# Kernel optimization log

Measured on AMD Instinct MI355X. Metric: run time of the kernel, lower is better.

## Reference

```python
import jax, jax.numpy as jnp
import numpy as np

TOP_K = 32
OBS_RADIUS = 1.0
N = 4096
IN_DIM = 4


def setup_inputs() -> dict:
    key = jax.random.key(0)
    ks = jax.random.split(key, 10)
    s = 0.05
    return {
        "states": jax.random.normal(ks[0], (N, 4), jnp.float32),
        "goals": jax.random.normal(ks[1], (N, 2), jnp.float32),
        "W1": jax.random.normal(ks[2], (64, IN_DIM + 1), jnp.float32) * s,
        "b1": jnp.zeros((64,), jnp.float32),
        "W2": jax.random.normal(ks[3], (128, 64), jnp.float32) * s,
        "b2": jnp.zeros((128,), jnp.float32),
        "Wd1": jax.random.normal(ks[4], (64, 132), jnp.float32) * s,
        "bd1": jnp.zeros((64,), jnp.float32),
        "Wd2": jax.random.normal(ks[5], (128, 64), jnp.float32) * s,
        "bd2": jnp.zeros((128,), jnp.float32),
        "Wd3": jax.random.normal(ks[6], (64, 128), jnp.float32) * s,
        "bd3": jnp.zeros((64,), jnp.float32),
        "Wd4": jax.random.normal(ks[7], (4, 64), jnp.float32) * s,
        "bd4": jnp.zeros((4,), jnp.float32),
    }


def reference(states, goals, W1, b1, W2, b2, Wd1, bd1, Wd2, bd2, Wd3, bd3, Wd4, bd4):
    n = states.shape[0]
    dt = states.dtype
    # pairwise relative states + one-hot self indicator -> [N, N, 5]
    x = states[:, None, :] - states[None, :, :]
    x = jnp.concatenate([x, jnp.eye(n, dtype=dt)[:, :, None]], axis=2)
    # remove_distant_agents: keep TOP_K nearest neighbors by planar distance
    d = jnp.sqrt(jnp.sum(x[:, :, :2] ** 2, axis=2) + 1e-4)  # [N, N]
    _, idx = jax.lax.top_k(-d, TOP_K)                        # [N, K]
    xk = jnp.take_along_axis(x, idx[:, :, None], axis=1)     # [N, K, 5]
    # observation-radius mask (torch reshape [N,K,1]->[N,1,K] == transpose here)
    dist = jnp.linalg.norm(xk[:, :, :2], axis=2)             # [N, K]
    mask = (dist < OBS_RADIUS).astype(dt).reshape(n, 1, TOP_K)
    # NOTE: original uses a raw reshape [N,K,5]->[N,5,K] (not a transpose); match it
    h = xk.reshape(n, IN_DIM + 1, TOP_K)
    # pointwise (kernel-1) conv stack 5 -> 64 -> 128
    h = jax.nn.relu(jnp.einsum('oc,ncp->nop', W1, h) + b1[None, :, None])
    h = jax.nn.relu(jnp.einsum('oc,ncp->nop', W2, h) + b2[None, :, None])
    # original does torch.max(...)[1]: ARGMAX indices, promoted to float by cat
    x_local = jnp.argmax(h * mask, axis=2).astype(dt)        # [N, 128]
    rel = states[:, :2] - goals
    feat = jnp.concatenate([x_local, rel, states[:, 2:]], axis=1)  # [N, 132]
    z = jax.nn.relu(feat @ Wd1.T + bd1)
    z = jax.nn.relu(z @ Wd2.T + bd2)
    z = jax.nn.relu(z @ Wd3.T + bd3)
    z = z @ Wd4.T + bd4
    k = 2.0 * jax.nn.sigmoid(z) + 0.2                        # [N, 4] gains
    state = jnp.concatenate([rel, states[:, 2:]], axis=1)    # [N, 4]
    a_x = -(k[:, 0] * state[:, 0] + k[:, 1] * state[:, 2])
    a_y = -(k[:, 2] * state[:, 1] + k[:, 3] * state[:, 3])
    return jnp.stack([a_x, a_y], axis=1)                     # [N, 2]
```

## Files before the change

### kernel.cpp

```cpp
#include <hip/hip_runtime.h>
#include <math.h>

#define NAGENT 4096
#define TOPK 32
#define AGB 4
#define DAGB 16
#define CANDCAP 2048

__global__ __launch_bounds__(256) void topk_kernel(
    const float* __restrict__ states, int* __restrict__ idx_out)
{
    const int i = blockIdx.x;
    const int t = threadIdx.x;
    __shared__ unsigned int hist[1024];
    __shared__ unsigned int ps[256];
    __shared__ unsigned int ps2[32];
    __shared__ unsigned long long cand[CANDCAP];
    __shared__ int ccount;
    __shared__ unsigned int cutB;

    #pragma unroll
    for (int u = 0; u < 4; ++u) hist[t + u * 256] = 0u;
    if (t == 0) ccount = 0;

    const float4 si = ((const float4*)states)[i];
    __syncthreads();

    unsigned int mybits[16];
    #pragma unroll
    for (int u = 0; u < 16; ++u) {
        int j = t + u * 256;
        float4 sj = ((const float4*)states)[j];
        float dx = __fsub_rn(si.x, sj.x);
        float dy = __fsub_rn(si.y, sj.y);
        float s  = __fadd_rn(__fadd_rn(__fmul_rn(dx, dx), __fmul_rn(dy, dy)), 1e-4f);
        float dv = sqrtf(s);
        mybits[u] = __float_as_uint(dv);
        unsigned int bin = (unsigned int)(dv * 256.0f);
        if (bin > 1023u) bin = 1023u;
        atomicAdd(&hist[bin], 1u);
    }
    __syncthreads();

    ps[t] = hist[t * 4 + 0] + hist[t * 4 + 1] + hist[t * 4 + 2] + hist[t * 4 + 3];
    __syncthreads();
    if (t < 32) {
        unsigned int s = 0;
        #pragma unroll
        for (int q = 0; q < 8; ++q) s += ps[t * 8 + q];
        ps2[t] = s;
    }
    __syncthreads();

    if (t == 0) {
        unsigned int cum = 0;
        int g2 = 0;
        while (cum + ps2[g2] < TOPK) { cum += ps2[g2]; ++g2; }
        int g1 = g2 * 8;
        while (cum + ps[g1] < TOPK) { cum += ps[g1]; ++g1; }
        int b = g1 * 4;
        for (;;) { cum += hist[b]; if (cum >= TOPK) break; ++b; }
        cutB = (unsigned int)b;
    }
    __syncthreads();

    const unsigned int B = cutB;
    #pragma unroll
    for (int u = 0; u < 16; ++u) {
        float dv = __uint_as_float(mybits[u]);
        unsigned int bin = (unsigned int)(dv * 256.0f);
        if (bin > 1023u) bin = 1023u;
        if (bin <= B) {
            int pos = atomicAdd(&ccount, 1);
            if (pos < CANDCAP)
                cand[pos] = ((unsigned long long)mybits[u] << 32)
                          | (unsigned int)(t + u * 256);
        }
    }
    __syncthreads();

    const int C = (ccount < CANDCAP) ? ccount : CANDCAP;
    for (int q = t; q < C; q += 256) {
        unsigned long long key = cand[q];
        int rank = 0;
        for (int r = 0; r < C; ++r) rank += (cand[r] < key) ? 1 : 0;
        if (rank < TOPK) idx_out[i * TOPK + rank] = (int)(key & 0xffffffffu);
    }
}

__global__ __launch_bounds__(256) void feat_kernel(
    const float* __restrict__ states, const float* __restrict__ goals,
    const float* __restrict__ W1, const float* __restrict__ b1,
    const float* __restrict__ W2, const float* __restrict__ b2,
    const int* __restrict__ idx_in, float* __restrict__ feat_ws)
{
    const int t = threadIdx.x;
    const int a = t >> 6;
    const int l = t & 63;
    const int i = blockIdx.x * AGB + a;

    __shared__ __attribute__((aligned(16))) float w2a[64 * 68];
    __shared__ __attribute__((aligned(16))) float w2b[64 * 68];
    __shared__ __attribute__((aligned(16))) float w1s[320];
    __shared__ __attribute__((aligned(16))) float b1s[64];
    __shared__ __attribute__((aligned(16))) float b2s[128];
    __shared__ __attribute__((aligned(16))) float flat[AGB][160];
    __shared__ __attribute__((aligned(16))) float maskv[AGB][32];
    __shared__ __attribute__((aligned(16))) float h1[AGB][2048];

    #pragma unroll
    for (int u = 0; u < 32; ++u) {
        int e = t + u * 256;
        int o = e >> 6, c = e & 63;
        float v = W2[e];
        int dst = c * 68 + ((o >> 3) << 2) + (o & 3);
        if (o & 4) w2b[dst] = v; else w2a[dst] = v;
    }
    for (int e = t; e < 320; e += 256) w1s[e] = W1[e];
    if (t < 64)  b1s[t] = b1[t];
    if (t < 128) b2s[t] = b2[t];

    if (l < 32) {
        int j = idx_in[i * TOPK + l];
        float4 sj  = ((const float4*)states)[j];
        float4 siv = ((const float4*)states)[i];
        float d0 = siv.x - sj.x;
        float d1 = siv.y - sj.y;
        float d2 = siv.z - sj.z;
        float d3 = siv.w - sj.w;
        flat[a][l * 5 + 0] = d0;
        flat[a][l * 5 + 1] = d1;
        flat[a][l * 5 + 2] = d2;
        flat[a][l * 5 + 3] = d3;
        flat[a][l * 5 + 4] = (j == i) ? 1.0f : 0.0f;
        float dist = sqrtf(__fadd_rn(__fmul_rn(d0, d0), __fmul_rn(d1, d1)));
        maskv[a][l] = (dist < 1.0f) ? 1.0f : 0.0f;
    } else if (l < 36) {
        int f = l - 32;
        float4 siv = ((const float4*)states)[i];
        float2 gi  = ((const float2*)goals)[i];
        float v = (f == 0) ? (siv.x - gi.x)
                : (f == 1) ? (siv.y - gi.y)
                : (f == 2) ? siv.z : siv.w;
        feat_ws[i * 132 + 128 + f] = v;
    }
    __syncthreads();

    #pragma unroll
    for (int u = 0; u < 32; ++u) {
        int e = u * 64 + l;
        int p = e & 31, o1 = e >> 5;
        float acc = b1s[o1];
        #pragma unroll
        for (int f = 0; f < 5; ++f)
            acc += w1s[o1 * 5 + f] * flat[a][f * 32 + p];
        h1[a][o1 * 32 + p] = fmaxf(acc, 0.0f);
    }
    __syncthreads();

    const int ow = l & 15;
    const int pt = l >> 4;
    float acc[8][8];
    #pragma unroll
    for (int k = 0; k < 8; ++k)
        #pragma unroll
        for (int q = 0; q < 8; ++q) acc[k][q] = 0.0f;

    for (int c = 0; c < 64; ++c) {
        float4 wA = *(const float4*)&w2a[c * 68 + ow * 4];
        float4 wB = *(const float4*)&w2b[c * 68 + ow * 4];
        float4 hA = *(const float4*)&h1[a][c * 32 + pt * 8];
        float4 hB = *(const float4*)&h1[a][c * 32 + pt * 8 + 4];
        float wv[8] = {wA.x, wA.y, wA.z, wA.w, wB.x, wB.y, wB.z, wB.w};
        float hv[8] = {hA.x, hA.y, hA.z, hA.w, hB.x, hB.y, hB.z, hB.w};
        #pragma unroll
        for (int k = 0; k < 8; ++k)
            #pragma unroll
            for (int q = 0; q < 8; ++q)
                acc[k][q] += wv[k] * hv[q];
    }

    float4 mA = *(const float4*)&maskv[a][pt * 8];
    float4 mB = *(const float4*)&maskv[a][pt * 8 + 4];
    float mv[8] = {mA.x, mA.y, mA.z, mA.w, mB.x, mB.y, mB.z, mB.w};
    #pragma unroll
    for (int k = 0; k < 8; ++k) {
        float bb = b2s[ow * 8 + k];
        unsigned long long best = 0ull;
        #pragma unroll
        for (int q = 0; q < 8; ++q) {
            float val = fmaxf(acc[k][q] + bb, 0.0f) * mv[q];
            unsigned long long key =
                ((unsigned long long)__float_as_uint(val) << 32)
                | (unsigned int)(31 - (pt * 8 + q));
            if (key > best) best = key;
        }
        unsigned long long o1 = __shfl_xor(best, 16, 64); if (o1 > best) best = o1;
        unsigned long long o2 = __shfl_xor(best, 32, 64); if (o2 > best) best = o2;
        if (pt == 0) {
            int pbest = 31 - (int)(best & 63ull);
            feat_ws[i * 132 + ow * 8 + k] = (float)pbest;
        }
    }
}

__global__ __launch_bounds__(256) void dense_kernel(
    const float* __restrict__ feat_ws,
    const float* __restrict__ Wd1, const float* __restrict__ bd1,
    const float* __restrict__ Wd2, const float* __restrict__ bd2,
    const float* __restrict__ Wd3, const float* __restrict__ bd3,
    const float* __restrict__ Wd4, const float* __restrict__ bd4,
    float* __restrict__ out)
{
    const int t = threadIdx.x;
    const int w = t >> 6;
    const int l = t & 63;
    const int A0 = blockIdx.x * DAGB;

    __shared__ __attribute__((aligned(16))) float fl[DAGB * 132];
    __shared__ __attribute__((aligned(16))) float z1[DAGB][64];
    __shared__ __attribute__((aligned(16))) float z2[DAGB][128];
    __shared__ __attribute__((aligned(16))) float z3[DAGB][64];
    __shared__ float kvs[DAGB][4];

    for (int e = t; e < DAGB * 132; e += 256) fl[e] = feat_ws[A0 * 132 + e];
    __syncthreads();

    const int gbase = w * 4;

    {
        float bb = bd1[l];
        float a0 = bb, a1 = bb, a2 = bb, a3 = bb;
        for (int k = 0; k < 33; ++k) {
            float4 wv = *(const float4*)&Wd1[l * 132 + 4 * k];
            float4 f0 = *(const float4*)&fl[(gbase + 0) * 132 + 4 * k];
            float4 f1 = *(const float4*)&fl[(gbase + 1) * 132 + 4 * k];
            float4 f2 = *(const float4*)&fl[(gbase + 2) * 132 + 4 * k];
            float4 f3 = *(const float4*)&fl[(gbase + 3) * 132 + 4 * k];
            a0 += wv.x * f0.x; a0 += wv.y * f0.y; a0 += wv.z * f0.z; a0 += wv.w * f0.w;
            a1 += wv.x * f1.x; a1 += wv.y * f1.y; a1 += wv.z * f1.z; a1 += wv.w * f1.w;
            a2 += wv.x * f2.x; a2 += wv.y * f2.y; a2 += wv.z * f2.z; a2 += wv.w * f2.w;
            a3 += wv.x * f3.x; a3 += wv.y * f3.y; a3 += wv.z * f3.z; a3 += wv.w * f3.w;
        }
        z1[gbase + 0][l] = fmaxf(a0, 0.0f);
        z1[gbase + 1][l] = fmaxf(a1, 0.0f);
        z1[gbase + 2][l] = fmaxf(a2, 0.0f);
        z1[gbase + 3][l] = fmaxf(a3, 0.0f);
    }

    {
        float accA[4], accB[4];
        float bA = bd2[l], bB = bd2[l + 64];
        #pragma unroll
        for (int g = 0; g < 4; ++g) { accA[g] = bA; accB[g] = bB; }
        for (int k = 0; k < 16; ++k) {
            float4 wa = *(const float4*)&Wd2[l * 64 + 4 * k];
            float4 wb = *(const float4*)&Wd2[(l + 64) * 64 + 4 * k];
            #pragma unroll
            for (int g = 0; g < 4; ++g) {
                float4 f = *(const float4*)&z1[gbase + g][4 * k];
                accA[g] += wa.x * f.x; accA[g] += wa.y * f.y;
                accA[g] += wa.z * f.z; accA[g] += wa.w * f.w;
                accB[g] += wb.x * f.x; accB[g] += wb.y * f.y;
                accB[g] += wb.z * f.z; accB[g] += wb.w * f.w;
            }
        }
        #pragma unroll
        for (int g = 0; g < 4; ++g) {
            z2[gbase + g][l]      = fmaxf(accA[g], 0.0f);
            z2[gbase + g][l + 64] = fmaxf(accB[g], 0.0f);
        }
    }

    {
        float acc[4];
        float bb = bd3[l];
        #pragma unroll
        for (int g = 0; g < 4; ++g) acc[g] = bb;
        for (int k = 0; k < 32; ++k) {
            float4 wv = *(const float4*)&Wd3[l * 128 + 4 * k];
            #pragma unroll
            for (int g = 0; g < 4; ++g) {
                float4 f = *(const float4*)&z2[gbase + g][4 * k];
                acc[g] += wv.x * f.x; acc[g] += wv.y * f.y;
                acc[g] += wv.z * f.z; acc[g] += wv.w * f.w;
            }
        }
        #pragma unroll
        for (int g = 0; g < 4; ++g) z3[gbase + g][l] = fmaxf(acc[g], 0.0f);
    }

    if (l < 16) {
        int g = l >> 2, o = l & 3;
        float acc = bd4[o];
        for (int c = 0; c < 64; ++c) acc += Wd4[o * 64 + c] * z3[gbase + g][c];
        kvs[gbase + g][o] = 2.0f / (1.0f + expf(-acc)) + 0.2f;
    }
    __syncthreads();

    if (l < 8) {
        int g = l >> 1, axis = l & 1;
        float ka = kvs[gbase + g][2 * axis + 0];
        float kb = kvs[gbase + g][2 * axis + 1];
        float rel = fl[(gbase + g) * 132 + 128 + axis];
        float vel = fl[(gbase + g) * 132 + 130 + axis];
        out[(A0 + gbase + g) * 2 + axis] = -(ka * rel + kb * vel);
    }
}

extern "C" void kernel_launch(void* const* d_in, const int* in_sizes, int n_in,
                              void* d_out, int out_size, void* d_ws, size_t ws_size,
                              hipStream_t stream)
{
    const float* states = (const float*)d_in[0];
    const float* goals  = (const float*)d_in[1];
    const float* W1  = (const float*)d_in[2];
    const float* b1  = (const float*)d_in[3];
    const float* W2  = (const float*)d_in[4];
    const float* b2  = (const float*)d_in[5];
    const float* Wd1 = (const float*)d_in[6];
    const float* bd1 = (const float*)d_in[7];
    const float* Wd2 = (const float*)d_in[8];
    const float* bd2 = (const float*)d_in[9];
    const float* Wd3 = (const float*)d_in[10];
    const float* bd3 = (const float*)d_in[11];
    const float* Wd4 = (const float*)d_in[12];
    const float* bd4 = (const float*)d_in[13];

    const size_t idx_bytes = (size_t)NAGENT * TOPK * 4;
    int*   idx     = (int*)d_ws;
    float* feat_ws = (float*)((char*)d_ws + idx_bytes);
    float* out     = (float*)d_out;

    topk_kernel<<<NAGENT, 256, 0, stream>>>(states, idx);
    feat_kernel<<<NAGENT / AGB, 256, 0, stream>>>(states, goals, W1, b1, W2, b2,
                                                  idx, feat_ws);
    dense_kernel<<<NAGENT / DAGB, 256, 0, stream>>>(feat_ws, Wd1, bd1, Wd2, bd2,
                                                    Wd3, bd3, Wd4, bd4, out);
}
```

Measured before the change: 152.5 us.

## Read conv weights directly from global memory and drop block barriers in feat_kernel

Stops staging W1, W2 and the biases into shared memory in every block and reads them straight from global memory, which should be served by cache. The W2 loop now loads 4 input channels of weights per output at a time as float4. The two block-wide barriers are removed, since each wave only touches its own agent's shared buffers, and the launch bounds now ask for more resident blocks. The aim is to cut the per-block weight copy and shared-memory footprint so more blocks fit per CU. In exchange, the W2 reads are strided and not coalesced, and correctness now relies on writes and reads within a single wave being ordered without an explicit barrier.

```diff
diff --git a/kernel.cpp b/kernel.cpp
--- a/kernel.cpp
+++ b/kernel.cpp
@@ -88,7 +88,7 @@
     }
 }
 
-__global__ __launch_bounds__(256) void feat_kernel(
+__global__ __launch_bounds__(256, 4) void feat_kernel(
     const float* __restrict__ states, const float* __restrict__ goals,
     const float* __restrict__ W1, const float* __restrict__ b1,
     const float* __restrict__ W2, const float* __restrict__ b2,
@@ -99,26 +99,9 @@
     const int l = t & 63;
     const int i = blockIdx.x * AGB + a;
 
-    __shared__ __attribute__((aligned(16))) float w2a[64 * 68];
-    __shared__ __attribute__((aligned(16))) float w2b[64 * 68];
-    __shared__ __attribute__((aligned(16))) float w1s[320];
-    __shared__ __attribute__((aligned(16))) float b1s[64];
-    __shared__ __attribute__((aligned(16))) float b2s[128];
     __shared__ __attribute__((aligned(16))) float flat[AGB][160];
     __shared__ __attribute__((aligned(16))) float maskv[AGB][32];
     __shared__ __attribute__((aligned(16))) float h1[AGB][2048];
-
-    #pragma unroll
-    for (int u = 0; u < 32; ++u) {
-        int e = t + u * 256;
-        int o = e >> 6, c = e & 63;
-        float v = W2[e];
-        int dst = c * 68 + ((o >> 3) << 2) + (o & 3);
-        if (o & 4) w2b[dst] = v; else w2a[dst] = v;
-    }
-    for (int e = t; e < 320; e += 256) w1s[e] = W1[e];
-    if (t < 64)  b1s[t] = b1[t];
-    if (t < 128) b2s[t] = b2[t];
 
     if (l < 32) {
         int j = idx_in[i * TOPK + l];
@@ -144,19 +127,17 @@
                 : (f == 2) ? siv.z : siv.w;
         feat_ws[i * 132 + 128 + f] = v;
     }
-    __syncthreads();
 
     #pragma unroll
     for (int u = 0; u < 32; ++u) {
         int e = u * 64 + l;
         int p = e & 31, o1 = e >> 5;
-        float acc = b1s[o1];
+        float acc = b1[o1];
         #pragma unroll
         for (int f = 0; f < 5; ++f)
-            acc += w1s[o1 * 5 + f] * flat[a][f * 32 + p];
+            acc += W1[o1 * 5 + f] * flat[a][f * 32 + p];
         h1[a][o1 * 32 + p] = fmaxf(acc, 0.0f);
     }
-    __syncthreads();
 
     const int ow = l & 15;
     const int pt = l >> 4;
@@ -166,18 +147,25 @@
         #pragma unroll
         for (int q = 0; q < 8; ++q) acc[k][q] = 0.0f;
 
-    for (int c = 0; c < 64; ++c) {
-        float4 wA = *(const float4*)&w2a[c * 68 + ow * 4];
-        float4 wB = *(const float4*)&w2b[c * 68 + ow * 4];
-        float4 hA = *(const float4*)&h1[a][c * 32 + pt * 8];
-        float4 hB = *(const float4*)&h1[a][c * 32 + pt * 8 + 4];
-        float wv[8] = {wA.x, wA.y, wA.z, wA.w, wB.x, wB.y, wB.z, wB.w};
-        float hv[8] = {hA.x, hA.y, hA.z, hA.w, hB.x, hB.y, hB.z, hB.w};
-        #pragma unroll
-        for (int k = 0; k < 8; ++k)
+    for (int c4 = 0; c4 < 16; ++c4) {
+        float w4[8][4];
+        #pragma unroll
+        for (int k = 0; k < 8; ++k) {
+            float4 wv = *(const float4*)&W2[(ow * 8 + k) * 64 + c4 * 4];
+            w4[k][0] = wv.x; w4[k][1] = wv.y; w4[k][2] = wv.z; w4[k][3] = wv.w;
+        }
+        #pragma unroll
+        for (int cc = 0; cc < 4; ++cc) {
+            int c = c4 * 4 + cc;
+            float4 hA = *(const float4*)&h1[a][c * 32 + pt * 8];
+            float4 hB = *(const float4*)&h1[a][c * 32 + pt * 8 + 4];
+            float hv[8] = {hA.x, hA.y, hA.z, hA.w, hB.x, hB.y, hB.z, hB.w};
             #pragma unroll
-            for (int q = 0; q < 8; ++q)
-                acc[k][q] += wv[k] * hv[q];
+            for (int k = 0; k < 8; ++k)
+                #pragma unroll
+                for (int q = 0; q < 8; ++q)
+                    acc[k][q] += w4[k][cc] * hv[q];
+        }
     }
 
     float4 mA = *(const float4*)&maskv[a][pt * 8];
@@ -185,7 +173,7 @@
     float mv[8] = {mA.x, mA.y, mA.z, mA.w, mB.x, mB.y, mB.z, mB.w};
     #pragma unroll
     for (int k = 0; k < 8; ++k) {
-        float bb = b2s[ow * 8 + k];
+        float bb = b2[ow * 8 + k];
         unsigned long long best = 0ull;
         #pragma unroll
         for (int q = 0; q < 8; ++q) {
```

New measurement: 189.0 us. 23.9% more time.

## Fuse feature and dense MLP kernels, processing eight agents per block

Applied to the files above, without the earlier changes.

Merges the per-agent conv/argmax feature kernel and the dense MLP kernel into one launch. Each block now handles eight agents in two rounds of four, so the W2 staging into shared memory is shared across twice as many agents. Features stay in shared memory instead of round-tripping through a global workspace, and one kernel launch is removed. In exchange, each wave now does the dense layers for only two agents, so the global Wd weight loads are reused less. Shared buffers are aliased for the dense intermediates, which relies on each wave touching only its own rows.

```diff
diff --git a/kernel.cpp b/kernel.cpp
--- a/kernel.cpp
+++ b/kernel.cpp
@@ -3,8 +3,7 @@
 
 #define NAGENT 4096
 #define TOPK 32
-#define AGB 4
-#define DAGB 16
+#define FAGB 8
 #define CANDCAP 2048
 
 __global__ __launch_bounds__(256) void topk_kernel(
@@ -88,25 +87,34 @@
     }
 }
 
-__global__ __launch_bounds__(256) void feat_kernel(
+__global__ __launch_bounds__(256) void fused_kernel(
     const float* __restrict__ states, const float* __restrict__ goals,
-    const float* __restrict__ W1, const float* __restrict__ b1,
-    const float* __restrict__ W2, const float* __restrict__ b2,
-    const int* __restrict__ idx_in, float* __restrict__ feat_ws)
+    const float* __restrict__ W1,  const float* __restrict__ b1,
+    const float* __restrict__ W2,  const float* __restrict__ b2,
+    const float* __restrict__ Wd1, const float* __restrict__ bd1,
+    const float* __restrict__ Wd2, const float* __restrict__ bd2,
+    const float* __restrict__ Wd3, const float* __restrict__ bd3,
+    const float* __restrict__ Wd4, const float* __restrict__ bd4,
+    const int* __restrict__ idx_in, float* __restrict__ out)
 {
     const int t = threadIdx.x;
     const int a = t >> 6;
     const int l = t & 63;
-    const int i = blockIdx.x * AGB + a;
+    const int base = blockIdx.x * FAGB;
 
     __shared__ __attribute__((aligned(16))) float w2a[64 * 68];
     __shared__ __attribute__((aligned(16))) float w2b[64 * 68];
     __shared__ __attribute__((aligned(16))) float w1s[320];
     __shared__ __attribute__((aligned(16))) float b1s[64];
     __shared__ __attribute__((aligned(16))) float b2s[128];
-    __shared__ __attribute__((aligned(16))) float flat[AGB][160];
-    __shared__ __attribute__((aligned(16))) float maskv[AGB][32];
-    __shared__ __attribute__((aligned(16))) float h1[AGB][2048];
+    __shared__ __attribute__((aligned(16))) float flat[4][160];
+    __shared__ __attribute__((aligned(16))) float maskv[4][32];
+    __shared__ __attribute__((aligned(16))) float featb[FAGB][132];
+    __shared__ __attribute__((aligned(16))) float h1[4][2048];
+    float* z1s = &h1[0][0];
+    float* z2s = z1s + 512;
+    float* z3s = z2s + 1024;
+    float* kvs = z3s + 512;
 
     #pragma unroll
     for (int u = 0; u < 32; ++u) {
@@ -119,192 +127,164 @@
     for (int e = t; e < 320; e += 256) w1s[e] = W1[e];
     if (t < 64)  b1s[t] = b1[t];
     if (t < 128) b2s[t] = b2[t];
-
-    if (l < 32) {
-        int j = idx_in[i * TOPK + l];
-        float4 sj  = ((const float4*)states)[j];
-        float4 siv = ((const float4*)states)[i];
-        float d0 = siv.x - sj.x;
-        float d1 = siv.y - sj.y;
-        float d2 = siv.z - sj.z;
-        float d3 = siv.w - sj.w;
-        flat[a][l * 5 + 0] = d0;
-        flat[a][l * 5 + 1] = d1;
-        flat[a][l * 5 + 2] = d2;
-        flat[a][l * 5 + 3] = d3;
-        flat[a][l * 5 + 4] = (j == i) ? 1.0f : 0.0f;
-        float dist = sqrtf(__fadd_rn(__fmul_rn(d0, d0), __fmul_rn(d1, d1)));
-        maskv[a][l] = (dist < 1.0f) ? 1.0f : 0.0f;
-    } else if (l < 36) {
-        int f = l - 32;
-        float4 siv = ((const float4*)states)[i];
-        float2 gi  = ((const float2*)goals)[i];
-        float v = (f == 0) ? (siv.x - gi.x)
-                : (f == 1) ? (siv.y - gi.y)
-                : (f == 2) ? siv.z : siv.w;
-        feat_ws[i * 132 + 128 + f] = v;
-    }
-    __syncthreads();
-
-    #pragma unroll
-    for (int u = 0; u < 32; ++u) {
-        int e = u * 64 + l;
-        int p = e & 31, o1 = e >> 5;
-        float acc = b1s[o1];
+    __syncthreads();
+
+    #pragma unroll
+    for (int round = 0; round < 2; ++round) {
+        const int g = round * 4 + a;
+        const int i = base + g;
+
+        if (l < 32) {
+            int j = idx_in[i * TOPK + l];
+            float4 sj  = ((const float4*)states)[j];
+            float4 siv = ((const float4*)states)[i];
+            float d0 = siv.x - sj.x;
+            float d1 = siv.y - sj.y;
+            float d2 = siv.z - sj.z;
+            float d3 = siv.w - sj.w;
+            flat[a][l * 5 + 0] = d0;
+            flat[a][l * 5 + 1] = d1;
+            flat[a][l * 5 + 2] = d2;
+            flat[a][l * 5 + 3] = d3;
+            flat[a][l * 5 + 4] = (j == i) ? 1.0f : 0.0f;
+            float dist = sqrtf(__fadd_rn(__fmul_rn(d0, d0), __fmul_rn(d1, d1)));
+            maskv[a][l] = (dist < 1.0f) ? 1.0f : 0.0f;
+        } else if (l < 36) {
+            int f = l - 32;
+            float4 siv = ((const float4*)states)[i];
+            float2 gi  = ((const float2*)goals)[i];
+            float v = (f == 0) ? (siv.x - gi.x)
+                    : (f == 1) ? (siv.y - gi.y)
+                    : (f == 2) ? siv.z : siv.w;
+            featb[g][128 + f] = v;
+        }
+
         #pragma unroll
-        for (int f = 0; f < 5; ++f)
-            acc += w1s[o1 * 5 + f] * flat[a][f * 32 + p];
-        h1[a][o1 * 32 + p] = fmaxf(acc, 0.0f);
-    }
-    __syncthreads();
-
-    const int ow = l & 15;
-    const int pt = l >> 4;
-    float acc[8][8];
-    #pragma unroll
-    for (int k = 0; k < 8; ++k)
-        #pragma unroll
-        for (int q = 0; q < 8; ++q) acc[k][q] = 0.0f;
-
-    for (int c = 0; c < 64; ++c) {
-        float4 wA = *(const float4*)&w2a[c * 68 + ow * 4];
-        float4 wB = *(const float4*)&w2b[c * 68 + ow * 4];
-        float4 hA = *(const float4*)&h1[a][c * 32 + pt * 8];
-        float4 hB = *(const float4*)&h1[a][c * 32 + pt * 8 + 4];
-        float wv[8] = {wA.x, wA.y, wA.z, wA.w, wB.x, wB.y, wB.z, wB.w};
-        float hv[8] = {hA.x, hA.y, hA.z, hA.w, hB.x, hB.y, hB.z, hB.w};
+        for (int u = 0; u < 32; ++u) {
+            int e = u * 64 + l;
+            int p = e & 31, o1 = e >> 5;
+            float acc = b1s[o1];
+            #pragma unroll
+            for (int f = 0; f < 5; ++f)
+                acc += w1s[o1 * 5 + f] * flat[a][f * 32 + p];
+            h1[a][o1 * 32 + p] = fmaxf(acc, 0.0f);
+        }
+
+        const int ow = l & 15;
+        const int pt = l >> 4;
+        float acc[8][8];
         #pragma unroll
         for (int k = 0; k < 8; ++k)
             #pragma unroll
-            for (int q = 0; q < 8; ++q)
-                acc[k][q] += wv[k] * hv[q];
-    }
-
-    float4 mA = *(const float4*)&maskv[a][pt * 8];
-    float4 mB = *(const float4*)&maskv[a][pt * 8 + 4];
-    float mv[8] = {mA.x, mA.y, mA.z, mA.w, mB.x, mB.y, mB.z, mB.w};
-    #pragma unroll
-    for (int k = 0; k < 8; ++k) {
-        float bb = b2s[ow * 8 + k];
-        unsigned long long best = 0ull;
+            for (int q = 0; q < 8; ++q) acc[k][q] = 0.0f;
+
+        for (int c = 0; c < 64; ++c) {
+            float4 wA = *(const float4*)&w2a[c * 68 + ow * 4];
+            float4 wB = *(const float4*)&w2b[c * 68 + ow * 4];
+            float4 hA = *(const float4*)&h1[a][c * 32 + pt * 8];
+            float4 hB = *(const float4*)&h1[a][c * 32 + pt * 8 + 4];
+            float wv[8] = {wA.x, wA.y, wA.z, wA.w, wB.x, wB.y, wB.z, wB.w};
+            float hv[8] = {hA.x, hA.y, hA.z, hA.w, hB.x, hB.y, hB.z, hB.w};
+            #pragma unroll
+            for (int k = 0; k < 8; ++k)
+                #pragma unroll
+                for (int q = 0; q < 8; ++q)
+                    acc[k][q] += wv[k] * hv[q];
+        }
+
+        float4 mA = *(const float4*)&maskv[a][pt * 8];
+        float4 mB = *(const float4*)&maskv[a][pt * 8 + 4];
+        float mv[8] = {mA.x, mA.y, mA.z, mA.w, mB.x, mB.y, mB.z, mB.w};
         #pragma unroll
-        for (int q = 0; q < 8; ++q) {
-            float val = fmaxf(acc[k][q] + bb, 0.0f) * mv[q];
-            unsigned long long key =
-                ((unsigned long long)__float_as_uint(val) << 32)
-                | (unsigned int)(31 - (pt * 8 + q));
-            if (key > best) best = key;
-        }
-        unsigned long long o1 = __shfl_xor(best, 16, 64); if (o1 > best) best = o1;
-        unsigned long long o2 = __shfl_xor(best, 32, 64); if (o2 > best) best = o2;
-        if (pt == 0) {
-            int pbest = 31 - (int)(best & 63ull);
-            feat_ws[i * 132 + ow * 8 + k] = (float)pbest;
-        }
-    }
-}
-
-__global__ __launch_bounds__(256) void dense_kernel(
-    const float* __restrict__ feat_ws,
-    const float* __restrict__ Wd1, const float* __restrict__ bd1,
-    const float* __restrict__ Wd2, const float* __restrict__ bd2,
-    const float* __restrict__ Wd3, const float* __restrict__ bd3,
-    const float* __restrict__ Wd4, const float* __restrict__ bd4,
-    float* __restrict__ out)
-{
-    const int t = threadIdx.x;
-    const int w = t >> 6;
-    const int l = t & 63;
-    const int A0 = blockIdx.x * DAGB;
-
-    __shared__ __attribute__((aligned(16))) float fl[DAGB * 132];
-    __shared__ __attribute__((aligned(16))) float z1[DAGB][64];
-    __shared__ __attribute__((aligned(16))) float z2[DAGB][128];
-    __shared__ __attribute__((aligned(16))) float z3[DAGB][64];
-    __shared__ float kvs[DAGB][4];
-
-    for (int e = t; e < DAGB * 132; e += 256) fl[e] = feat_ws[A0 * 132 + e];
-    __syncthreads();
-
-    const int gbase = w * 4;
+        for (int k = 0; k < 8; ++k) {
+            float bb = b2s[ow * 8 + k];
+            unsigned long long best = 0ull;
+            #pragma unroll
+            for (int q = 0; q < 8; ++q) {
+                float val = fmaxf(acc[k][q] + bb, 0.0f) * mv[q];
+                unsigned long long key =
+                    ((unsigned long long)__float_as_uint(val) << 32)
+                    | (unsigned int)(31 - (pt * 8 + q));
+                if (key > best) best = key;
+            }
+            unsigned long long o1 = __shfl_xor(best, 16, 64); if (o1 > best) best = o1;
+            unsigned long long o2 = __shfl_xor(best, 32, 64); if (o2 > best) best = o2;
+            if (pt == 0) {
+                int pbest = 31 - (int)(best & 63ull);
+                featb[g][ow * 8 + k] = (float)pbest;
+            }
+        }
+    }
+    __syncthreads();
+
+    const int g0 = 2 * a, g1 = 2 * a + 1;
 
     {
         float bb = bd1[l];
-        float a0 = bb, a1 = bb, a2 = bb, a3 = bb;
+        float a0 = bb, a1 = bb;
         for (int k = 0; k < 33; ++k) {
             float4 wv = *(const float4*)&Wd1[l * 132 + 4 * k];
-            float4 f0 = *(const float4*)&fl[(gbase + 0) * 132 + 4 * k];
-            float4 f1 = *(const float4*)&fl[(gbase + 1) * 132 + 4 * k];
-            float4 f2 = *(const float4*)&fl[(gbase + 2) * 132 + 4 * k];
-            float4 f3 = *(const float4*)&fl[(gbase + 3) * 132 + 4 * k];
+            float4 f0 = *(const float4*)&featb[g0][4 * k];
+            float4 f1 = *(const float4*)&featb[g1][4 * k];
             a0 += wv.x * f0.x; a0 += wv.y * f0.y; a0 += wv.z * f0.z; a0 += wv.w * f0.w;
             a1 += wv.x * f1.x; a1 += wv.y * f1.y; a1 += wv.z * f1.z; a1 += wv.w * f1.w;
-            a2 += wv.x * f2.x; a2 += wv.y * f2.y; a2 += wv.z * f2.z; a2 += wv.w * f2.w;
-            a3 += wv.x * f3.x; a3 += wv.y * f3.y; a3 += wv.z * f3.z; a3 += wv.w * f3.w;
-        }
-        z1[gbase + 0][l] = fmaxf(a0, 0.0f);
-        z1[gbase + 1][l] = fmaxf(a1, 0.0f);
-        z1[gbase + 2][l] = fmaxf(a2, 0.0f);
-        z1[gbase + 3][l] = fmaxf(a3, 0.0f);
+        }
+        z1s[g0 * 64 + l] = fmaxf(a0, 0.0f);
+        z1s[g1 * 64 + l] = fmaxf(a1, 0.0f);
     }
 
     {
-        float accA[4], accB[4];
-        float bA = bd2[l], bB = bd2[l + 64];
-        #pragma unroll
-        for (int g = 0; g < 4; ++g) { accA[g] = bA; accB[g] = bB; }
+        float accA0 = bd2[l], accA1 = bd2[l];
+        float accB0 = bd2[l + 64], accB1 = bd2[l + 64];
         for (int k = 0; k < 16; ++k) {
             float4 wa = *(const float4*)&Wd2[l * 64 + 4 * k];
             float4 wb = *(const float4*)&Wd2[(l + 64) * 64 + 4 * k];
-            #pragma unroll
-            for (int g = 0; g < 4; ++g) {
-                float4 f = *(const float4*)&z1[gbase + g][4 * k];
-                accA[g] += wa.x * f.x; accA[g] += wa.y * f.y;
-                accA[g] += wa.z * f.z; accA[g] += wa.w * f.w;
-                accB[g] += wb.x * f.x; accB[g] += wb.y * f.y;
-                accB[g] += wb.z * f.z; accB[g] += wb.w * f.w;
-            }
-        }
-        #pragma unroll
-        for (int g = 0; g < 4; ++g) {
-            z2[gbase + g][l]      = fmaxf(accA[g], 0.0f);
-            z2[gbase + g][l + 64] = fmaxf(accB[g], 0.0f);
-        }
+            float4 f0 = *(const float4*)&z1s[g0 * 64 + 4 * k];
+            float4 f1 = *(const float4*)&z1s[g1 * 64 + 4 * k];
+            accA0 += wa.x * f0.x; accA0 += wa.y * f0.y;
+            accA0 += wa.z * f0.z; accA0 += wa.w * f0.w;
+            accB0 += wb.x * f0.x; accB0 += wb.y * f0.y;
+            accB0 += wb.z * f0.z; accB0 += wb.w * f0.w;
+            accA1 += wa.x * f1.x; accA1 += wa.y * f1.y;
+            accA1 += wa.z * f1.z; accA1 += wa.w * f1.w;
+            accB1 += wb.x * f1.x; accB1 += wb.y * f1.y;
+            accB1 += wb.z * f1.z; accB1 += wb.w * f1.w;
+        }
+        z2s[g0 * 128 + l]      = fmaxf(accA0, 0.0f);
+        z2s[g0 * 128 + l + 64] = fmaxf(accB0, 0.0f);
+        z2s[g1 * 128 + l]      = fmaxf(accA1, 0.0f);
+        z2s[g1 * 128 + l + 64] = fmaxf(accB1, 0.0f);
     }
 
     {
-        float acc[4];
         float bb = bd3[l];
-        #pragma unroll
-        for (int g = 0; g < 4; ++g) acc[g] = bb;
+        float a0 = bb, a1 = bb;
         for (int k = 0; k < 32; ++k) {
             float4 wv = *(const float4*)&Wd3[l * 128 + 4 * k];
-            #pragma unroll
-            for (int g = 0; g < 4; ++g) {
-                float4 f = *(const float4*)&z2[gbase + g][4 * k];
-                acc[g] += wv.x * f.x; acc[g] += wv.y * f.y;
-                acc[g] += wv.z * f.z; acc[g] += wv.w * f.w;
-            }
-        }
-        #pragma unroll
-        for (int g = 0; g < 4; ++g) z3[gbase + g][l] = fmaxf(acc[g], 0.0f);
-    }
-
-    if (l < 16) {
-        int g = l >> 2, o = l & 3;
+            float4 f0 = *(const float4*)&z2s[g0 * 128 + 4 * k];
+            float4 f1 = *(const float4*)&z2s[g1 * 128 + 4 * k];
+            a0 += wv.x * f0.x; a0 += wv.y * f0.y; a0 += wv.z * f0.z; a0 += wv.w * f0.w;
+            a1 += wv.x * f1.x; a1 += wv.y * f1.y; a1 += wv.z * f1.z; a1 += wv.w * f1.w;
+        }
+        z3s[g0 * 64 + l] = fmaxf(a0, 0.0f);
+        z3s[g1 * 64 + l] = fmaxf(a1, 0.0f);
+    }
+
+    if (l < 8) {
+        int gg = (l >> 2) ? g1 : g0;
+        int o = l & 3;
         float acc = bd4[o];
-        for (int c = 0; c < 64; ++c) acc += Wd4[o * 64 + c] * z3[gbase + g][c];
-        kvs[gbase + g][o] = 2.0f / (1.0f + expf(-acc)) + 0.2f;
-    }
-    __syncthreads();
-
-    if (l < 8) {
-        int g = l >> 1, axis = l & 1;
-        float ka = kvs[gbase + g][2 * axis + 0];
-        float kb = kvs[gbase + g][2 * axis + 1];
-        float rel = fl[(gbase + g) * 132 + 128 + axis];
-        float vel = fl[(gbase + g) * 132 + 130 + axis];
-        out[(A0 + gbase + g) * 2 + axis] = -(ka * rel + kb * vel);
+        for (int c = 0; c < 64; ++c) acc += Wd4[o * 64 + c] * z3s[gg * 64 + c];
+        kvs[gg * 4 + o] = 2.0f / (1.0f + expf(-acc)) + 0.2f;
+    }
+    if (l < 4) {
+        int gg = (l >> 1) ? g1 : g0;
+        int axis = l & 1;
+        float ka = kvs[gg * 4 + 2 * axis + 0];
+        float kb = kvs[gg * 4 + 2 * axis + 1];
+        float rel = featb[gg][128 + axis];
+        float vel = featb[gg][130 + axis];
+        out[(base + gg) * 2 + axis] = -(ka * rel + kb * vel);
     }
 }
 
@@ -327,14 +307,11 @@
     const float* Wd4 = (const float*)d_in[12];
     const float* bd4 = (const float*)d_in[13];
 
-    const size_t idx_bytes = (size_t)NAGENT * TOPK * 4;
-    int*   idx     = (int*)d_ws;
-    float* feat_ws = (float*)((char*)d_ws + idx_bytes);
-    float* out     = (float*)d_out;
+    int*   idx = (int*)d_ws;
+    float* out = (float*)d_out;
 
     topk_kernel<<<NAGENT, 256, 0, stream>>>(states, idx);
-    feat_kernel<<<NAGENT / AGB, 256, 0, stream>>>(states, goals, W1, b1, W2, b2,
-                                                  idx, feat_ws);
-    dense_kernel<<<NAGENT / DAGB, 256, 0, stream>>>(feat_ws, Wd1, bd1, Wd2, bd2,
-                                                    Wd3, bd3, Wd4, bd4, out);
+    fused_kernel<<<NAGENT / FAGB, 256, 0, stream>>>(states, goals, W1, b1, W2, b2,
+                                                    Wd1, bd1, Wd2, bd2, Wd3, bd3,
+                                                    Wd4, bd4, idx, out);
 }
```

Result: faster. 141.5 us (-7.2%).
